# Optimization experiments

Measured on AMD Instinct MI355X. Metric: run time of the kernel, lower is better.

Reference implementation:

```python
import jax, jax.numpy as jnp
import numpy as np

EMBED_DIM = 768
NUM_HEADS = 12
HEAD_DIM = EMBED_DIM // NUM_HEADS


def setup_inputs() -> dict:
    key = jax.random.key(0)
    ks = jax.random.split(key, 9)
    B, S, D = 2, 2048, EMBED_DIM
    scale = 1.0 / np.sqrt(D)
    x = jax.random.normal(ks[0], (B, S, D), dtype=jnp.float32)
    Wq = jax.random.normal(ks[1], (D, D), dtype=jnp.float32) * scale
    bq = jax.random.normal(ks[2], (D,), dtype=jnp.float32) * 0.01
    Wk = jax.random.normal(ks[3], (D, D), dtype=jnp.float32) * scale
    bk = jax.random.normal(ks[4], (D,), dtype=jnp.float32) * 0.01
    Wv = jax.random.normal(ks[5], (D, D), dtype=jnp.float32) * scale
    bv = jax.random.normal(ks[6], (D,), dtype=jnp.float32) * 0.01
    Wo = jax.random.normal(ks[7], (D, D), dtype=jnp.float32) * scale
    bo = jax.random.normal(ks[8], (D,), dtype=jnp.float32) * 0.01
    return {"x": x, "Wq": Wq, "bq": bq, "Wk": Wk, "bk": bk,
            "Wv": Wv, "bv": bv, "Wo": Wo, "bo": bo}


def reference(x, Wq, bq, Wk, bk, Wv, bv, Wo, bo):
    B, S, D = x.shape
    H, hd = NUM_HEADS, HEAD_DIM
    # projections (torch Linear: x @ W^T + b; here W stored as (D,D) used directly)
    q = (x @ Wq + bq).reshape(B, S, H, hd).transpose(0, 2, 1, 3)  # (B,H,S,hd)
    k = (x @ Wk + bk).reshape(B, S, H, hd).transpose(0, 2, 1, 3)
    v = (x @ Wv + bv).reshape(B, S, H, hd).transpose(0, 2, 1, 3)
    scores = jnp.einsum('bhqd,bhkd->bhqk', q, k) / jnp.sqrt(jnp.float32(hd))
    attn = jax.nn.softmax(scores, axis=-1)                        # (B,H,S,S)
    out = jnp.einsum('bhqk,bhkd->bhqd', attn, v)                  # (B,H,S,hd)
    out = out.transpose(0, 2, 1, 3).reshape(B, S, D)
    return out @ Wo + bo
```

## Files before the change

### kernel.cpp

```cpp
#include <hip/hip_runtime.h>
#include <hip/hip_bf16.h>

#define NHEADS 12
#define HDIM 64
#define BATCH 2
#define SEQ 2048
#define DMODEL 768
#define MROWS (BATCH * SEQ)

typedef __bf16  bf16x8 __attribute__((ext_vector_type(8)));
typedef float   f32x4  __attribute__((ext_vector_type(4)));

__device__ inline unsigned short to_bf16(float f) {
    union { float f; unsigned u; } x; x.f = f;
    const unsigned r = x.u + 0x7FFFu + ((x.u >> 16) & 1u);
    return (unsigned short)(r >> 16);
}
__device__ inline unsigned pack_bf16x2(float a, float b) {
    const __hip_bfloat162 h = __float22bfloat162_rn(float2{a, b});
    union { __hip_bfloat162 h; unsigned u; } c; c.h = h; return c.u;
}

#define GLDS16(gsrc, ldst)                                                    \
    __builtin_amdgcn_global_load_lds(                                         \
        (const __attribute__((address_space(1))) void*)(gsrc),                \
        (__attribute__((address_space(3))) void*)(ldst), 16, 0, 0)

__global__ __launch_bounds__(256) void cvt_x(const float* __restrict__ in,
                                             unsigned short* __restrict__ out,
                                             int n4) {
    const int i = blockIdx.x * 256 + threadIdx.x;
    if (i < n4) {
        const float4 v = reinterpret_cast<const float4*>(in)[i];
        ushort4 o;
        o.x = to_bf16(v.x); o.y = to_bf16(v.y);
        o.z = to_bf16(v.z); o.w = to_bf16(v.w);
        reinterpret_cast<ushort4*>(out)[i] = o;
    }
}

__global__ __launch_bounds__(256) void cvt_wT(const float* __restrict__ Wq,
                                              const float* __restrict__ Wk,
                                              const float* __restrict__ Wv,
                                              const float* __restrict__ Wo,
                                              unsigned short* __restrict__ wt_all,
                                              unsigned short* __restrict__ wot) {
    const int z = blockIdx.z;
    const float* W = (z == 0) ? Wq : (z == 1) ? Wk : (z == 2) ? Wv : Wo;
    unsigned short* out = (z < 3) ? (wt_all + (size_t)z * DMODEL * DMODEL) : wot;

    __shared__ float tile[32][33];
    const int tx = threadIdx.x & 31, ty = threadIdx.x >> 5;
    const int nbase = blockIdx.x * 32, kbase = blockIdx.y * 32;

    #pragma unroll
    for (int p = 0; p < 4; ++p) {
        const int r = ty + p * 8;
        tile[r][tx] = W[(size_t)(kbase + r) * DMODEL + nbase + tx];
    }
    __syncthreads();
    #pragma unroll
    for (int p = 0; p < 4; ++p) {
        const int r = ty + p * 8;
        out[(size_t)(nbase + r) * DMODEL + kbase + tx] = to_bf16(tile[tx][r]);
    }
}

__global__ __launch_bounds__(256) void gemm_qkv(const unsigned short* __restrict__ A,
                                                const unsigned short* __restrict__ Wt,
                                                const float* __restrict__ bq,
                                                const float* __restrict__ bk,
                                                const float* __restrict__ bv,
                                                unsigned short* __restrict__ q_bf,
                                                unsigned short* __restrict__ k_bf,
                                                unsigned short* __restrict__ vt_bf) {
    constexpr int K = DMODEL;
    __shared__ unsigned short As[128 * 32];
    __shared__ unsigned short Bs[128 * 32];

    const int t = threadIdx.x;
    const int lane = t & 63;
    const int w = t >> 6, wr = w >> 1, wc = w & 1;
    const int m0 = blockIdx.y * 128, n0 = blockIdx.x * 128;
    const int lr = lane & 15;
    const int kg = lane >> 4;

    const int row0 = t >> 2,        cp0 = t & 3;
    const int row1 = (t + 256) >> 2, cp1 = t & 3;
    const int c0 = cp0 ^ ((row0 >> 1) & 3);
    const int c1 = cp1 ^ ((row1 >> 1) & 3);
    unsigned short* asd0 = &As[(w * 64) * 8];
    unsigned short* asd1 = &As[(256 + w * 64) * 8];
    unsigned short* bsd0 = &Bs[(w * 64) * 8];
    unsigned short* bsd1 = &Bs[(256 + w * 64) * 8];

    f32x4 acc[4][4] = {};

    for (int k0 = 0; k0 < K; k0 += 32) {
        GLDS16(A  + (size_t)(m0 + row0) * K + k0 + c0 * 8, asd0);
        GLDS16(A  + (size_t)(m0 + row1) * K + k0 + c1 * 8, asd1);
        GLDS16(Wt + (size_t)(n0 + row0) * K + k0 + c0 * 8, bsd0);
        GLDS16(Wt + (size_t)(n0 + row1) * K + k0 + c1 * 8, bsd1);
        __syncthreads();

        bf16x8 af[4], bfr[4];
        #pragma unroll
        for (int i = 0; i < 4; ++i) {
            const int ar = wr * 64 + i * 16 + lr;
            af[i] = *reinterpret_cast<const bf16x8*>(
                &As[ar * 32 + ((kg ^ ((ar >> 1) & 3)) * 8)]);
            const int br = wc * 64 + i * 16 + lr;
            bfr[i] = *reinterpret_cast<const bf16x8*>(
                &Bs[br * 32 + ((kg ^ ((br >> 1) & 3)) * 8)]);
        }
        #pragma unroll
        for (int i = 0; i < 4; ++i)
            #pragma unroll
            for (int j = 0; j < 4; ++j)
                acc[i][j] = __builtin_amdgcn_mfma_f32_16x16x32_bf16(
                    af[i], bfr[j], acc[i][j], 0, 0, 0);
        __syncthreads();
    }

    const int seg = n0 / DMODEL;
    const float scale = (seg == 0) ? 0.125f : 1.0f;
    const float* bias = (seg == 0) ? bq : (seg == 1) ? bk : bv;
    const int mb = m0 + wr * 64, nb = n0 - seg * DMODEL + wc * 64;

    #pragma unroll
    for (int i = 0; i < 4; ++i) {
        #pragma unroll
        for (int j = 0; j < 4; ++j) {
            const int cl = nb + j * 16 + lr;
            const float bv_ = bias[cl];
            const int h = cl >> 6, d = cl & (HDIM - 1);
            if (seg < 2) {
                unsigned short* dst = (seg == 0) ? q_bf : k_bf;
                #pragma unroll
                for (int q = 0; q < 4; ++q) {
                    const int row = mb + i * 16 + kg * 4 + q;
                    const int b = row >> 11, s = row & (SEQ - 1);
                    dst[(((size_t)(b * NHEADS + h)) * SEQ + s) * HDIM + d] =
                        to_bf16((acc[i][j][q] + bv_) * scale);
                }
            } else {
                ushort4 pk;
                #pragma unroll
                for (int q = 0; q < 4; ++q)
                    ((unsigned short*)&pk)[q] = to_bf16(acc[i][j][q] + bv_);
                const int r0 = mb + i * 16 + kg * 4;
                const int b = r0 >> 11, s = r0 & (SEQ - 1);
                *reinterpret_cast<ushort4*>(
                    &vt_bf[(((size_t)(b * NHEADS + h)) * HDIM + d) * SEQ + s]) = pk;
            }
        }
    }
}

__global__ __launch_bounds__(256) void gemm_out(const unsigned short* __restrict__ A,
                                                const unsigned short* __restrict__ Bt,
                                                const float* __restrict__ bias,
                                                float* __restrict__ out) {
    constexpr int K = DMODEL;
    __shared__ unsigned short As[128 * 32];
    __shared__ unsigned short Bs[128 * 32];

    const int t = threadIdx.x;
    const int lane = t & 63;
    const int w = t >> 6, wr = w >> 1, wc = w & 1;
    const int m0 = blockIdx.y * 128, n0 = blockIdx.x * 128;
    const int lr = lane & 15;
    const int kg = lane >> 4;

    const int row0 = t >> 2,        cp0 = t & 3;
    const int row1 = (t + 256) >> 2, cp1 = t & 3;
    const int c0 = cp0 ^ ((row0 >> 1) & 3);
    const int c1 = cp1 ^ ((row1 >> 1) & 3);
    unsigned short* asd0 = &As[(w * 64) * 8];
    unsigned short* asd1 = &As[(256 + w * 64) * 8];
    unsigned short* bsd0 = &Bs[(w * 64) * 8];
    unsigned short* bsd1 = &Bs[(256 + w * 64) * 8];

    f32x4 acc[4][4] = {};

    for (int k0 = 0; k0 < K; k0 += 32) {
        GLDS16(A  + (size_t)(m0 + row0) * K + k0 + c0 * 8, asd0);
        GLDS16(A  + (size_t)(m0 + row1) * K + k0 + c1 * 8, asd1);
        GLDS16(Bt + (size_t)(n0 + row0) * K + k0 + c0 * 8, bsd0);
        GLDS16(Bt + (size_t)(n0 + row1) * K + k0 + c1 * 8, bsd1);
        __syncthreads();

        bf16x8 af[4], bfr[4];
        #pragma unroll
        for (int i = 0; i < 4; ++i) {
            const int ar = wr * 64 + i * 16 + lr;
            af[i] = *reinterpret_cast<const bf16x8*>(
                &As[ar * 32 + ((kg ^ ((ar >> 1) & 3)) * 8)]);
            const int br = wc * 64 + i * 16 + lr;
            bfr[i] = *reinterpret_cast<const bf16x8*>(
                &Bs[br * 32 + ((kg ^ ((br >> 1) & 3)) * 8)]);
        }
        #pragma unroll
        for (int i = 0; i < 4; ++i)
            #pragma unroll
            for (int j = 0; j < 4; ++j)
                acc[i][j] = __builtin_amdgcn_mfma_f32_16x16x32_bf16(
                    af[i], bfr[j], acc[i][j], 0, 0, 0);
        __syncthreads();
    }

    const int mb = m0 + wr * 64, nb = n0 + wc * 64;
    #pragma unroll
    for (int i = 0; i < 4; ++i) {
        #pragma unroll
        for (int j = 0; j < 4; ++j) {
            const int col = nb + j * 16 + lr;
            const float bv = bias[col];
            #pragma unroll
            for (int q = 0; q < 4; ++q) {
                const int row = mb + i * 16 + kg * 4 + q;
                out[(size_t)row * DMODEL + col] = acc[i][j][q] + bv;
            }
        }
    }
}

__global__ __launch_bounds__(256, 4) void flash_mfma(
        const unsigned short* __restrict__ Qg,
        const unsigned short* __restrict__ Kgl,
        const unsigned short* __restrict__ Vtg,
        unsigned short* __restrict__ Cctx) {
    __shared__ __align__(16) unsigned short k_s[64 * 72];
    __shared__ __align__(16) unsigned short v_s[64 * 72];
    __shared__ __align__(16) unsigned short p_s[4 * 16 * 72];

    const int t = threadIdx.x;
    const int lane = t & 63, w = t >> 6;
    const int lr = lane & 15, kg = lane >> 4;
    const int qb = blockIdx.x, bh = blockIdx.y;
    const size_t sbase = (size_t)bh * SEQ * HDIM;
    const size_t vtb   = (size_t)bh * HDIM * SEQ;

    const int q0 = qb * 64 + w * 16;
    const bf16x8 qf0 = *reinterpret_cast<const bf16x8*>(
        &Qg[sbase + (size_t)(q0 + lr) * HDIM + kg * 8]);
    const bf16x8 qf1 = *reinterpret_cast<const bf16x8*>(
        &Qg[sbase + (size_t)(q0 + lr) * HDIM + 32 + kg * 8]);

    bf16x8 ones;
    #pragma unroll
    for (int i = 0; i < 8; ++i) ones[i] = (__bf16)1.0f;

    const int sr = t >> 2, cst = t & 3;

    uint4 kr0, kr1, vr0, vr1;
    {
        const size_t ka = sbase + (size_t)sr * HDIM;
        kr0 = *reinterpret_cast<const uint4*>(&Kgl[ka + cst * 8]);
        kr1 = *reinterpret_cast<const uint4*>(&Kgl[ka + (cst + 4) * 8]);
        const size_t va = vtb + (size_t)sr * SEQ;
        vr0 = *reinterpret_cast<const uint4*>(&Vtg[va + cst * 8]);
        vr1 = *reinterpret_cast<const uint4*>(&Vtg[va + (cst + 4) * 8]);
    }

    f32x4 oa[4] = {};
    f32x4 l_acc = {};
    float m_run[4] = {-1e30f, -1e30f, -1e30f, -1e30f};

    const int NT = SEQ / 64;
    for (int kt = 0; kt < NT; ++kt) {
        __syncthreads();
        *reinterpret_cast<uint4*>(&k_s[sr * 72 + cst * 8])       = kr0;
        *reinterpret_cast<uint4*>(&k_s[sr * 72 + (cst + 4) * 8]) = kr1;
        *reinterpret_cast<uint4*>(&v_s[sr * 72 + cst * 8])       = vr0;
        *reinterpret_cast<uint4*>(&v_s[sr * 72 + (cst + 4) * 8]) = vr1;
        __syncthreads();
        if (kt + 1 < NT) {
            const size_t ka = sbase + (size_t)((kt + 1) * 64 + sr) * HDIM;
            kr0 = *reinterpret_cast<const uint4*>(&Kgl[ka + cst * 8]);
            kr1 = *reinterpret_cast<const uint4*>(&Kgl[ka + (cst + 4) * 8]);
            const size_t va = vtb + (size_t)sr * SEQ + (kt + 1) * 64;
            vr0 = *reinterpret_cast<const uint4*>(&Vtg[va + cst * 8]);
            vr1 = *reinterpret_cast<const uint4*>(&Vtg[va + (cst + 4) * 8]);
        }

        f32x4 st[4] = {};
        __builtin_amdgcn_s_setprio(1);
        #pragma unroll
        for (int jk = 0; jk < 4; ++jk) {
            const bf16x8 kf0 = *reinterpret_cast<const bf16x8*>(
                &k_s[(jk * 16 + lr) * 72 + kg * 8]);
            const bf16x8 kf1 = *reinterpret_cast<const bf16x8*>(
                &k_s[(jk * 16 + lr) * 72 + 32 + kg * 8]);
            st[jk] = __builtin_amdgcn_mfma_f32_16x16x32_bf16(qf0, kf0, st[jk], 0, 0, 0);
            st[jk] = __builtin_amdgcn_mfma_f32_16x16x32_bf16(qf1, kf1, st[jk], 0, 0, 0);
        }
        __builtin_amdgcn_s_setprio(0);

        float mx[4];
        #pragma unroll
        for (int q = 0; q < 4; ++q)
            mx[q] = fmaxf(fmaxf(st[0][q], st[1][q]), fmaxf(st[2][q], st[3][q]));
        #pragma unroll
        for (int s = 1; s < 16; s <<= 1)
            #pragma unroll
            for (int q = 0; q < 4; ++q)
                mx[q] = fmaxf(mx[q], __shfl_xor(mx[q], s));

        float f[4];
        #pragma unroll
        for (int q = 0; q < 4; ++q) {
            const float mn = fmaxf(m_run[q], mx[q]);
            f[q] = __expf(m_run[q] - mn);
            m_run[q] = mn;
        }

        unsigned pk01[4], pk23[4];
        #pragma unroll
        for (int jk = 0; jk < 4; ++jk) {
            pk01[jk] = pack_bf16x2(__expf(st[jk][0] - m_run[0]),
                                   __expf(st[jk][1] - m_run[1]));
            pk23[jk] = pack_bf16x2(__expf(st[jk][2] - m_run[2]),
                                   __expf(st[jk][3] - m_run[3]));
        }

        #pragma unroll
        for (int q = 0; q < 4; ++q) l_acc[q] *= f[q];
        #pragma unroll
        for (int jd = 0; jd < 4; ++jd)
            #pragma unroll
            for (int q = 0; q < 4; ++q)
                oa[jd][q] *= f[q];

        const int pbase = w * (16 * 72);
        #pragma unroll
        for (int jk = 0; jk < 4; ++jk) {
            p_s[pbase + (kg * 4 + 0) * 72 + jk * 16 + lr] = (unsigned short)(pk01[jk] & 0xFFFFu);
            p_s[pbase + (kg * 4 + 1) * 72 + jk * 16 + lr] = (unsigned short)(pk01[jk] >> 16);
            p_s[pbase + (kg * 4 + 2) * 72 + jk * 16 + lr] = (unsigned short)(pk23[jk] & 0xFFFFu);
            p_s[pbase + (kg * 4 + 3) * 72 + jk * 16 + lr] = (unsigned short)(pk23[jk] >> 16);
        }
        const bf16x8 pf0 = *reinterpret_cast<const bf16x8*>(
            &p_s[pbase + lr * 72 + kg * 8]);
        const bf16x8 pf1 = *reinterpret_cast<const bf16x8*>(
            &p_s[pbase + lr * 72 + 32 + kg * 8]);

        __builtin_amdgcn_s_setprio(1);
        l_acc = __builtin_amdgcn_mfma_f32_16x16x32_bf16(pf0, ones, l_acc, 0, 0, 0);
        l_acc = __builtin_amdgcn_mfma_f32_16x16x32_bf16(pf1, ones, l_acc, 0, 0, 0);
        #pragma unroll
        for (int jd = 0; jd < 4; ++jd) {
            const bf16x8 vf0 = *reinterpret_cast<const bf16x8*>(
                &v_s[(jd * 16 + lr) * 72 + kg * 8]);
            const bf16x8 vf1 = *reinterpret_cast<const bf16x8*>(
                &v_s[(jd * 16 + lr) * 72 + 32 + kg * 8]);
            oa[jd] = __builtin_amdgcn_mfma_f32_16x16x32_bf16(pf0, vf0, oa[jd], 0, 0, 0);
            oa[jd] = __builtin_amdgcn_mfma_f32_16x16x32_bf16(pf1, vf1, oa[jd], 0, 0, 0);
        }
        __builtin_amdgcn_s_setprio(0);
    }

    const int b = bh / NHEADS, h = bh % NHEADS;
    #pragma unroll
    for (int q = 0; q < 4; ++q) {
        const float inv = 1.0f / l_acc[q];
        const int s = q0 + kg * 4 + q;
        #pragma unroll
        for (int jd = 0; jd < 4; ++jd)
            Cctx[(size_t)(b * SEQ + s) * DMODEL + h * HDIM + jd * 16 + lr] =
                to_bf16(oa[jd][q] * inv);
    }
}

extern "C" void kernel_launch(void* const* d_in, const int* in_sizes, int n_in,
                              void* d_out, int out_size, void* d_ws, size_t ws_size,
                              hipStream_t stream) {
    const float* x  = (const float*)d_in[0];
    const float* Wq = (const float*)d_in[1];
    const float* bq = (const float*)d_in[2];
    const float* Wk = (const float*)d_in[3];
    const float* bk = (const float*)d_in[4];
    const float* Wv = (const float*)d_in[5];
    const float* bv = (const float*)d_in[6];
    const float* Wo = (const float*)d_in[7];
    const float* bo = (const float*)d_in[8];
    float* out = (float*)d_out;

    const size_t MD = (size_t)MROWS * DMODEL;
    const size_t W2 = (size_t)DMODEL * DMODEL;
    unsigned short* u = (unsigned short*)d_ws;
    unsigned short* x_bf   = u;
    unsigned short* q_bf   = u + MD;
    unsigned short* k_bf   = u + 2 * MD;
    unsigned short* vt_bf  = u + 3 * MD;
    unsigned short* c_bf   = u + 4 * MD;
    unsigned short* wt_all = u + 5 * MD;
    unsigned short* wot    = wt_all + 3 * W2;

    cvt_x<<<(int)(MD / 4 + 255) / 256, 256, 0, stream>>>(x, x_bf, (int)(MD / 4));
    cvt_wT<<<dim3(24, 24, 4), 256, 0, stream>>>(Wq, Wk, Wv, Wo, wt_all, wot);

    dim3 gq(3 * DMODEL / 128, MROWS / 128);
    gemm_qkv<<<gq, 256, 0, stream>>>(x_bf, wt_all, bq, bk, bv, q_bf, k_bf, vt_bf);

    dim3 ga(SEQ / 64, BATCH * NHEADS);
    flash_mfma<<<ga, 256, 0, stream>>>(q_bf, k_bf, vt_bf, c_bf);

    dim3 gg(DMODEL / 128, MROWS / 128);
    gemm_out<<<gg, 256, 0, stream>>>(c_bf, wot, bo, out);
}
```

Baseline: 214.7 us.

## Merge convert kernels, shrink out-proj tiles, load V fragments directly from global

Three separate changes. The two fp32-to-bf16 conversion kernels become one launch that dispatches on block index, removing one kernel launch. The output-projection GEMM tile shrinks from 128x128 to 64x64, raising the block count from 192 to 768 so more CUs are busy, at the cost of less operand reuse per block. The flash attention kernel drops the V shared-memory staging and loads V^T fragments straight from global memory into registers each iteration. That frees LDS and one set of stores, but the loads are no longer prefetched a tile ahead, and the occupancy hint falls from 4 to 3 blocks.

```diff
diff --git a/kernel.cpp b/kernel.cpp
--- a/kernel.cpp
+++ b/kernel.cpp
@@ -26,32 +26,33 @@
         (const __attribute__((address_space(1))) void*)(gsrc),                \
         (__attribute__((address_space(3))) void*)(ldst), 16, 0, 0)
 
-__global__ __launch_bounds__(256) void cvt_x(const float* __restrict__ in,
-                                             unsigned short* __restrict__ out,
-                                             int n4) {
-    const int i = blockIdx.x * 256 + threadIdx.x;
-    if (i < n4) {
-        const float4 v = reinterpret_cast<const float4*>(in)[i];
+__global__ __launch_bounds__(256) void cvt_all(const float* __restrict__ x,
+                                               const float* __restrict__ Wq,
+                                               const float* __restrict__ Wk,
+                                               const float* __restrict__ Wv,
+                                               const float* __restrict__ Wo,
+                                               unsigned short* __restrict__ x_bf,
+                                               unsigned short* __restrict__ wt_all,
+                                               unsigned short* __restrict__ wot) {
+    __shared__ float tile[32][33];
+    const int bid = blockIdx.x;
+    if (bid < 3072) {
+        const int i = bid * 256 + threadIdx.x;
+        const float4 v = reinterpret_cast<const float4*>(x)[i];
         ushort4 o;
         o.x = to_bf16(v.x); o.y = to_bf16(v.y);
         o.z = to_bf16(v.z); o.w = to_bf16(v.w);
-        reinterpret_cast<ushort4*>(out)[i] = o;
-    }
-}
-
-__global__ __launch_bounds__(256) void cvt_wT(const float* __restrict__ Wq,
-                                              const float* __restrict__ Wk,
-                                              const float* __restrict__ Wv,
-                                              const float* __restrict__ Wo,
-                                              unsigned short* __restrict__ wt_all,
-                                              unsigned short* __restrict__ wot) {
-    const int z = blockIdx.z;
+        reinterpret_cast<ushort4*>(x_bf)[i] = o;
+        return;
+    }
+    const int wz = bid - 3072;
+    const int z = wz / 576, r2 = wz % 576;
+    const int bx = r2 % 24, by = r2 / 24;
     const float* W = (z == 0) ? Wq : (z == 1) ? Wk : (z == 2) ? Wv : Wo;
     unsigned short* out = (z < 3) ? (wt_all + (size_t)z * DMODEL * DMODEL) : wot;
 
-    __shared__ float tile[32][33];
     const int tx = threadIdx.x & 31, ty = threadIdx.x >> 5;
-    const int nbase = blockIdx.x * 32, kbase = blockIdx.y * 32;
+    const int nbase = bx * 32, kbase = by * 32;
 
     #pragma unroll
     for (int p = 0; p < 4; ++p) {
@@ -162,76 +163,69 @@
                                                 const float* __restrict__ bias,
                                                 float* __restrict__ out) {
     constexpr int K = DMODEL;
-    __shared__ unsigned short As[128 * 32];
-    __shared__ unsigned short Bs[128 * 32];
+    __shared__ unsigned short As[64 * 32];
+    __shared__ unsigned short Bs[64 * 32];
 
     const int t = threadIdx.x;
     const int lane = t & 63;
     const int w = t >> 6, wr = w >> 1, wc = w & 1;
-    const int m0 = blockIdx.y * 128, n0 = blockIdx.x * 128;
+    const int m0 = blockIdx.y * 64, n0 = blockIdx.x * 64;
     const int lr = lane & 15;
     const int kg = lane >> 4;
 
-    const int row0 = t >> 2,        cp0 = t & 3;
-    const int row1 = (t + 256) >> 2, cp1 = t & 3;
-    const int c0 = cp0 ^ ((row0 >> 1) & 3);
-    const int c1 = cp1 ^ ((row1 >> 1) & 3);
-    unsigned short* asd0 = &As[(w * 64) * 8];
-    unsigned short* asd1 = &As[(256 + w * 64) * 8];
-    unsigned short* bsd0 = &Bs[(w * 64) * 8];
-    unsigned short* bsd1 = &Bs[(256 + w * 64) * 8];
-
-    f32x4 acc[4][4] = {};
+    const int row = t >> 2, cp = t & 3;
+    const int c = cp ^ ((row >> 1) & 3);
+    unsigned short* asd = &As[(w * 16) * 32];
+    unsigned short* bsd = &Bs[(w * 16) * 32];
+
+    f32x4 acc[2][2] = {};
 
     for (int k0 = 0; k0 < K; k0 += 32) {
-        GLDS16(A  + (size_t)(m0 + row0) * K + k0 + c0 * 8, asd0);
-        GLDS16(A  + (size_t)(m0 + row1) * K + k0 + c1 * 8, asd1);
-        GLDS16(Bt + (size_t)(n0 + row0) * K + k0 + c0 * 8, bsd0);
-        GLDS16(Bt + (size_t)(n0 + row1) * K + k0 + c1 * 8, bsd1);
-        __syncthreads();
-
-        bf16x8 af[4], bfr[4];
-        #pragma unroll
-        for (int i = 0; i < 4; ++i) {
-            const int ar = wr * 64 + i * 16 + lr;
+        GLDS16(A  + (size_t)(m0 + row) * K + k0 + c * 8, asd);
+        GLDS16(Bt + (size_t)(n0 + row) * K + k0 + c * 8, bsd);
+        __syncthreads();
+
+        bf16x8 af[2], bfr[2];
+        #pragma unroll
+        for (int i = 0; i < 2; ++i) {
+            const int ar = wr * 32 + i * 16 + lr;
             af[i] = *reinterpret_cast<const bf16x8*>(
                 &As[ar * 32 + ((kg ^ ((ar >> 1) & 3)) * 8)]);
-            const int br = wc * 64 + i * 16 + lr;
+            const int br = wc * 32 + i * 16 + lr;
             bfr[i] = *reinterpret_cast<const bf16x8*>(
                 &Bs[br * 32 + ((kg ^ ((br >> 1) & 3)) * 8)]);
         }
         #pragma unroll
-        for (int i = 0; i < 4; ++i)
-            #pragma unroll
-            for (int j = 0; j < 4; ++j)
+        for (int i = 0; i < 2; ++i)
+            #pragma unroll
+            for (int j = 0; j < 2; ++j)
                 acc[i][j] = __builtin_amdgcn_mfma_f32_16x16x32_bf16(
                     af[i], bfr[j], acc[i][j], 0, 0, 0);
         __syncthreads();
     }
 
-    const int mb = m0 + wr * 64, nb = n0 + wc * 64;
-    #pragma unroll
-    for (int i = 0; i < 4; ++i) {
-        #pragma unroll
-        for (int j = 0; j < 4; ++j) {
+    const int mb = m0 + wr * 32, nb = n0 + wc * 32;
+    #pragma unroll
+    for (int i = 0; i < 2; ++i) {
+        #pragma unroll
+        for (int j = 0; j < 2; ++j) {
             const int col = nb + j * 16 + lr;
             const float bv = bias[col];
             #pragma unroll
             for (int q = 0; q < 4; ++q) {
-                const int row = mb + i * 16 + kg * 4 + q;
-                out[(size_t)row * DMODEL + col] = acc[i][j][q] + bv;
+                const int row2 = mb + i * 16 + kg * 4 + q;
+                out[(size_t)row2 * DMODEL + col] = acc[i][j][q] + bv;
             }
         }
     }
 }
 
-__global__ __launch_bounds__(256, 4) void flash_mfma(
+__global__ __launch_bounds__(256, 3) void flash_mfma(
         const unsigned short* __restrict__ Qg,
         const unsigned short* __restrict__ Kgl,
         const unsigned short* __restrict__ Vtg,
         unsigned short* __restrict__ Cctx) {
     __shared__ __align__(16) unsigned short k_s[64 * 72];
-    __shared__ __align__(16) unsigned short v_s[64 * 72];
     __shared__ __align__(16) unsigned short p_s[4 * 16 * 72];
 
     const int t = threadIdx.x;
@@ -253,14 +247,11 @@
 
     const int sr = t >> 2, cst = t & 3;
 
-    uint4 kr0, kr1, vr0, vr1;
+    uint4 kr0, kr1;
     {
         const size_t ka = sbase + (size_t)sr * HDIM;
         kr0 = *reinterpret_cast<const uint4*>(&Kgl[ka + cst * 8]);
         kr1 = *reinterpret_cast<const uint4*>(&Kgl[ka + (cst + 4) * 8]);
-        const size_t va = vtb + (size_t)sr * SEQ;
-        vr0 = *reinterpret_cast<const uint4*>(&Vtg[va + cst * 8]);
-        vr1 = *reinterpret_cast<const uint4*>(&Vtg[va + (cst + 4) * 8]);
     }
 
     f32x4 oa[4] = {};
@@ -272,16 +263,20 @@
         __syncthreads();
         *reinterpret_cast<uint4*>(&k_s[sr * 72 + cst * 8])       = kr0;
         *reinterpret_cast<uint4*>(&k_s[sr * 72 + (cst + 4) * 8]) = kr1;
-        *reinterpret_cast<uint4*>(&v_s[sr * 72 + cst * 8])       = vr0;
-        *reinterpret_cast<uint4*>(&v_s[sr * 72 + (cst + 4) * 8]) = vr1;
-        __syncthreads();
+        __syncthreads();
+
+        bf16x8 vf[4][2];
+        #pragma unroll
+        for (int jd = 0; jd < 4; ++jd)
+            #pragma unroll
+            for (int h2 = 0; h2 < 2; ++h2)
+                vf[jd][h2] = *reinterpret_cast<const bf16x8*>(
+                    &Vtg[vtb + (size_t)(jd * 16 + lr) * SEQ + kt * 64 + h2 * 32 + kg * 8]);
+
         if (kt + 1 < NT) {
             const size_t ka = sbase + (size_t)((kt + 1) * 64 + sr) * HDIM;
             kr0 = *reinterpret_cast<const uint4*>(&Kgl[ka + cst * 8]);
             kr1 = *reinterpret_cast<const uint4*>(&Kgl[ka + (cst + 4) * 8]);
-            const size_t va = vtb + (size_t)sr * SEQ + (kt + 1) * 64;
-            vr0 = *reinterpret_cast<const uint4*>(&Vtg[va + cst * 8]);
-            vr1 = *reinterpret_cast<const uint4*>(&Vtg[va + (cst + 4) * 8]);
         }
 
         f32x4 st[4] = {};
@@ -350,12 +345,8 @@
         l_acc = __builtin_amdgcn_mfma_f32_16x16x32_bf16(pf1, ones, l_acc, 0, 0, 0);
         #pragma unroll
         for (int jd = 0; jd < 4; ++jd) {
-            const bf16x8 vf0 = *reinterpret_cast<const bf16x8*>(
-                &v_s[(jd * 16 + lr) * 72 + kg * 8]);
-            const bf16x8 vf1 = *reinterpret_cast<const bf16x8*>(
-                &v_s[(jd * 16 + lr) * 72 + 32 + kg * 8]);
-            oa[jd] = __builtin_amdgcn_mfma_f32_16x16x32_bf16(pf0, vf0, oa[jd], 0, 0, 0);
-            oa[jd] = __builtin_amdgcn_mfma_f32_16x16x32_bf16(pf1, vf1, oa[jd], 0, 0, 0);
+            oa[jd] = __builtin_amdgcn_mfma_f32_16x16x32_bf16(pf0, vf[jd][0], oa[jd], 0, 0, 0);
+            oa[jd] = __builtin_amdgcn_mfma_f32_16x16x32_bf16(pf1, vf[jd][1], oa[jd], 0, 0, 0);
         }
         __builtin_amdgcn_s_setprio(0);
     }
@@ -397,8 +388,8 @@
     unsigned short* wt_all = u + 5 * MD;
     unsigned short* wot    = wt_all + 3 * W2;
 
-    cvt_x<<<(int)(MD / 4 + 255) / 256, 256, 0, stream>>>(x, x_bf, (int)(MD / 4));
-    cvt_wT<<<dim3(24, 24, 4), 256, 0, stream>>>(Wq, Wk, Wv, Wo, wt_all, wot);
+    cvt_all<<<3072 + 4 * 576, 256, 0, stream>>>(x, Wq, Wk, Wv, Wo,
+                                                x_bf, wt_all, wot);
 
     dim3 gq(3 * DMODEL / 128, MROWS / 128);
     gemm_qkv<<<gq, 256, 0, stream>>>(x_bf, wt_all, bq, bk, bv, q_bf, k_bf, vt_bf);
@@ -406,6 +397,6 @@
     dim3 ga(SEQ / 64, BATCH * NHEADS);
     flash_mfma<<<ga, 256, 0, stream>>>(q_bf, k_bf, vt_bf, c_bf);
 
-    dim3 gg(DMODEL / 128, MROWS / 128);
-    gemm_out<<<gg, 256, 0, stream>>>(c_bf, wot, bo, out);
-}
+    dim3 go(DMODEL / 64, MROWS / 64);
+    gemm_out<<<go, 256, 0, stream>>>(c_bf, wot, bo, out);
+}
```

Result: slower. 233.6 us (+8.8%).
